# Performance work log

Hardware: AMD Instinct MI355X
Metric: run time of the kernel (lower is better)

Reference implementation:

```python
import jax, jax.numpy as jnp
import numpy as np

NUM_HEADS = 12


def setup_inputs() -> dict:
    key = jax.random.key(0)
    k1, k2, k3 = jax.random.split(key, 3)
    B, N, C = 2, 2048, 768
    x = jax.random.normal(k1, (B, N, C), dtype=jnp.float32)
    # torch nn.Linear weights: [out_features, in_features]
    w_qkv = jax.random.normal(k2, (3 * C, C), dtype=jnp.float32) * (C ** -0.5)
    w_mlp = jax.random.normal(k3, (C, C), dtype=jnp.float32) * (C ** -0.5)
    b_mlp = jnp.zeros((C,), dtype=jnp.float32)
    return {"x": x, "w_qkv": w_qkv, "w_mlp": w_mlp, "b_mlp": b_mlp}


def reference(x, w_qkv, w_mlp, b_mlp):
    B, N, C = x.shape
    H = NUM_HEADS
    hd = C // H
    scale = hd ** -0.5
    # qkv linear (no bias), then the module's reshape: [B,N,H,3,hd]
    qkv = (x @ w_qkv.T).reshape(B, N, H, 3, hd)
    # permute(3,0,2,1,4) -> q,k,v each [B,H,N,hd]
    q = jnp.transpose(qkv[:, :, :, 0, :], (0, 2, 1, 3))
    k = jnp.transpose(qkv[:, :, :, 1, :], (0, 2, 1, 3))
    v = jnp.transpose(qkv[:, :, :, 2, :], (0, 2, 1, 3))
    attn = jax.nn.softmax(jnp.einsum('bhqd,bhkd->bhqk', q, k) * scale, axis=-1)
    out = jnp.einsum('bhqk,bhkd->bhqd', attn, v)          # [B,H,N,hd]
    out = jnp.transpose(out, (0, 2, 1, 3)).reshape(B, N, C)
    return out @ w_mlp.T + b_mlp
```

## Files before the change

### kernel.cpp

```cpp
#include <hip/hip_runtime.h>
#include <math.h>

typedef unsigned short u16;
typedef unsigned int   u32;
typedef __attribute__((ext_vector_type(8))) short s8v;
typedef __attribute__((ext_vector_type(4))) float f4v;
typedef __attribute__((ext_vector_type(16))) float f16v;

#define NHEADS 12
#define SEQ 2048
#define CD 768
#define BB 2
#define QKVD 2304
#define CEXP 0.18033688f
#define DEFER_THR 44.0f

__device__ inline u16 f2bf(float f) {
    union { float f; unsigned u; } v; v.f = f;
    unsigned r = v.u + 0x7FFFu + ((v.u >> 16) & 1u);
    return (u16)(r >> 16);
}
__device__ inline u32 cvtpk_bf16(float lo, float hi) {
    u32 r;
    asm("v_cvt_pk_bf16_f32 %0, %1, %2" : "=v"(r) : "v"(lo), "v"(hi));
    return r;
}
__device__ inline float exp2_fast(float x) {
    float r;
    asm("v_exp_f32 %0, %1" : "=v"(r) : "v"(x));
    return r;
}
__device__ inline float max3f(float a, float b, float c) {
    float r;
    asm("v_max3_f32 %0, %1, %2, %3" : "=v"(r) : "v"(a), "v"(b), "v"(c));
    return r;
}

#define GLOAD16(SRC, DST) __builtin_amdgcn_global_load_lds(                 \
    (const __attribute__((address_space(1))) void*)(SRC),                   \
    (__attribute__((address_space(3))) void*)(DST), 16, 0, 0)

#define SW(r, c) ((((r) << 6) + (c)) ^ (((r) & 7) << 3))
#define SW16(r, c) ((((r) << 7) + (c)) ^ (((r) & 15) << 3))

__global__ __launch_bounds__(256)
void cvt3_kernel(const float* __restrict__ a, u16* __restrict__ oa, int na,
                 const float* __restrict__ b, u16* __restrict__ ob, int nb,
                 const float* __restrict__ c, u16* __restrict__ oc) {
    const int i = (blockIdx.x * 256 + threadIdx.x) * 8;
    const float* src; u16* dst;
    if (i < na)           { src = a + i;            dst = oa + i; }
    else if (i < na + nb) { src = b + (i - na);     dst = ob + (i - na); }
    else                  { src = c + (i - na - nb); dst = oc + (i - na - nb); }
    const float4 x = *(const float4*)src;
    const float4 y = *(const float4*)(src + 4);
    s8v o;
    o[0] = (short)f2bf(x.x); o[1] = (short)f2bf(x.y);
    o[2] = (short)f2bf(x.z); o[3] = (short)f2bf(x.w);
    o[4] = (short)f2bf(y.x); o[5] = (short)f2bf(y.y);
    o[6] = (short)f2bf(y.z); o[7] = (short)f2bf(y.w);
    *(s8v*)dst = o;
}

template<int BN, int NBX, bool OUT_BF16, bool BIAS>
__global__ __launch_bounds__(256)
void gemm_bf16(const u16* __restrict__ A, const u16* __restrict__ W,
               const float* __restrict__ bias, void* __restrict__ Cout,
               int M, int N, int K) {
    constexpr int NF = BN / 32;
    __shared__ u16 As[8192];
    __shared__ u16 Bs[BN * 64];
    const int tid = threadIdx.x;
    const int l  = tid & 63, w = tid >> 6;
    const int wr = w >> 1, wc = w & 1;
    const int lq = l & 15, lg = l >> 4;

    const int fid = blockIdx.x;
    const int cpx = gridDim.x >> 3;
    const int swz = (fid & 7) * cpx + (fid >> 3);
    const int rowBase = (swz / NBX) << 7;
    const int colBase = (swz % NBX) * BN;

    f4v acc[4][NF];
    #pragma unroll
    for (int m = 0; m < 4; ++m)
        #pragma unroll
        for (int n = 0; n < NF; ++n)
            #pragma unroll
            for (int r = 0; r < 4; ++r) acc[m][n][r] = 0.f;

    const int chunk = l & 7;
    const int r8    = l >> 3;

    for (int kb = 0; kb < K; kb += 64) {
        __syncthreads();
        #pragma unroll
        for (int j = 0; j < 4; ++j) {
            const int rowA = (w << 5) + (j << 3) + r8;
            const int sc   = (chunk ^ (rowA & 7)) << 3;
            GLOAD16(A + (size_t)(rowBase + rowA) * K + kb + sc,
                    &As[(w << 11) + (j << 9)]);
        }
        #pragma unroll
        for (int j = 0; j < NF; ++j) {
            const int rowB = w * (BN / 4) + (j << 3) + r8;
            const int sc   = (chunk ^ (rowB & 7)) << 3;
            GLOAD16(W + (size_t)(colBase + rowB) * K + kb + sc,
                    &Bs[w * (BN * 16) + (j << 9)]);
        }
        __syncthreads();
        #pragma unroll
        for (int h = 0; h < 2; ++h) {
            const int kc = (h << 5) + (lg << 3);
            s8v af[4], bf[NF];
            #pragma unroll
            for (int m = 0; m < 4; ++m)
                af[m] = *(const s8v*)&As[SW((wr << 6) + (m << 4) + lq, kc)];
            #pragma unroll
            for (int n = 0; n < NF; ++n)
                bf[n] = *(const s8v*)&Bs[SW(wc * (BN / 2) + (n << 4) + lq, kc)];
            #pragma unroll
            for (int m = 0; m < 4; ++m)
                #pragma unroll
                for (int n = 0; n < NF; ++n)
                    acc[m][n] = __builtin_amdgcn_mfma_f32_16x16x32_bf16(
                        af[m], bf[n], acc[m][n], 0, 0, 0);
        }
    }

    #pragma unroll
    for (int m = 0; m < 4; ++m)
        #pragma unroll
        for (int r = 0; r < 4; ++r) {
            const int row = rowBase + (wr << 6) + (m << 4) + (lg << 2) + r;
            #pragma unroll
            for (int n = 0; n < NF; ++n) {
                const int col = colBase + wc * (BN / 2) + (n << 4) + lq;
                float v = acc[m][n][r];
                if (BIAS) v += bias[col];
                if (OUT_BF16) ((u16*)Cout)[(size_t)row * N + col] = f2bf(v);
                else        ((float*)Cout)[(size_t)row * N + col] = v;
            }
        }
}

__global__ __launch_bounds__(256)
void vtrans_kernel(const u16* __restrict__ qkvb, u16* __restrict__ vT) {
    __shared__ u16 T[64][66];
    const int bh = blockIdx.y;
    const int tt = blockIdx.x;
    const int b = bh / NHEADS, h = bh % NHEADS;
    const int r  = threadIdx.x >> 2;
    const int dc = (threadIdx.x & 3) << 4;
    const u16* src = qkvb + (size_t)(b * SEQ + tt * 64 + r) * QKVD
                   + h * 192 + 128 + dc;
    *(s8v*)&T[r][dc]     = *(const s8v*)(src);
    *(s8v*)&T[r][dc + 8] = *(const s8v*)(src + 8);
    __syncthreads();
    const int d  = threadIdx.x >> 2;
    const int tc = (threadIdx.x & 3) << 4;
    s8v o0, o1;
    #pragma unroll
    for (int j = 0; j < 8; ++j) {
        o0[j] = (short)T[tc + j][d];
        o1[j] = (short)T[tc + 8 + j][d];
    }
    u16* dst = vT + ((size_t)bh * 64 + d) * SEQ + tt * 64 + tc;
    *(s8v*)dst = o0;
    *(s8v*)(dst + 8) = o1;
}

__global__ __launch_bounds__(256)
void attn_mfma(const u16* __restrict__ qkv, const u16* __restrict__ vT,
               u16* __restrict__ outb) {
    __shared__ u16 SL[20480];
    __shared__ float ML[128];
    const int tid = threadIdx.x;
    const int l  = tid & 63, w = tid >> 6;
    const int g  = w >> 1, wl = w & 1;
    const int lq = l & 31;
    const int lh = l >> 5;

    const int fid = blockIdx.x;
    const int swz = (fid & 7) * 96 + (fid >> 3);
    const int q0 = (swz & 31) << 6;
    const int bh = swz >> 5;
    const int b = bh / NHEADS, hh = bh % NHEADS;
    const u16* base  = qkv + (size_t)b * SEQ * QKVD + hh * 192;
    const u16* baseK = base + 64;
    const u16* vbh   = vT + (size_t)bh * 64 * SEQ;

    const int kv0 = g << 10;
    u16* Kl = SL + (g << 13);
    u16* Vl = Kl + 4096;
    u16* Ql = SL + 16384;
    float* Of32 = (float*)(SL + 8192);
    float* Msh = ML;
    float* Lsh = ML + 64;
    u16* Ot = SL + 16384;

    u32 kso[4], vso[4];
    #pragma unroll
    for (int i = 0; i < 4; ++i) {
        const int r  = (wl << 4) + (i << 2) + (l >> 4);
        const int cg = (l & 15) ^ (r & 15);
        const int kk = ((cg >> 3) << 5) + r;
        const int cc = (cg & 7) << 3;
        kso[i] = (u32)((kv0 + kk) * QKVD + cc);
        vso[i] = (u32)(kk * SEQ + kv0 + cc);
    }

    {
        #pragma unroll
        for (int i = 0; i < 4; ++i) {
            GLOAD16(baseK + kso[i], &Kl[(wl << 11) + (i << 9)]);
            GLOAD16(vbh  + vso[i], &Vl[(wl << 11) + (i << 9)]);
        }
        const int qr = tid >> 3, qc = (tid & 7) << 3;
        const s8v qv0 = *(const s8v*)(base + (size_t)(q0 + qr) * QKVD + qc);
        const s8v qv1 = *(const s8v*)(base + (size_t)(q0 + 32 + qr) * QKVD + qc);
        *(s8v*)&Ql[SW16(qr, qc)]      = qv0;
        *(s8v*)&Ql[SW16(qr, 64 + qc)] = qv1;
    }
    __syncthreads();

    s8v qf[4];
    #pragma unroll
    for (int ds = 0; ds < 4; ++ds)
        qf[ds] = *(const s8v*)&Ql[SW16(lq, (wl << 6) + (ds << 4) + (lh << 3))];

    f16v z16;
    #pragma unroll
    for (int r = 0; r < 16; ++r) z16[r] = 0.f;
    f16v oa0 = z16, oa1 = z16;
    float osum = 0.f, mrun = -3.0e38f;

    for (int t = 0; t < 16; ++t) {
        s8v ka[8];
        #pragma unroll
        for (int kb = 0; kb < 2; ++kb)
            #pragma unroll
            for (int ds = 0; ds < 4; ++ds)
                ka[kb * 4 + ds] = *(const s8v*)
                    &Kl[SW16(lq, (kb << 6) + (ds << 4) + (lh << 3))];
        f16v s0 = z16, s1 = z16;
        __builtin_amdgcn_s_setprio(1);
        #pragma unroll
        for (int ds = 0; ds < 4; ++ds)
            s0 = __builtin_amdgcn_mfma_f32_32x32x16_bf16(ka[ds], qf[ds], s0, 0, 0, 0);
        #pragma unroll
        for (int ds = 0; ds < 4; ++ds)
            s1 = __builtin_amdgcn_mfma_f32_32x32x16_bf16(ka[4 + ds], qf[ds], s1, 0, 0, 0);
        __builtin_amdgcn_s_setprio(0);

        __syncthreads();
        if (t < 15) {
            const u16* sb = baseK + (size_t)(t + 1) * (64 * QKVD);
            #pragma unroll
            for (int i = 0; i < 4; ++i)
                GLOAD16(sb + kso[i], &Kl[(wl << 11) + (i << 9)]);
        }

        float mxa = max3f(s0[0], s0[1], s0[2]);
        mxa = max3f(mxa, s0[3], s0[4]);  mxa = max3f(mxa, s0[5], s0[6]);
        mxa = max3f(mxa, s0[7], s0[8]);  mxa = max3f(mxa, s0[9], s0[10]);
        mxa = max3f(mxa, s0[11], s0[12]); mxa = max3f(mxa, s0[13], s0[14]);
        float mxb = max3f(s1[0], s1[1], s1[2]);
        mxb = max3f(mxb, s1[3], s1[4]);  mxb = max3f(mxb, s1[5], s1[6]);
        mxb = max3f(mxb, s1[7], s1[8]);  mxb = max3f(mxb, s1[9], s1[10]);
        mxb = max3f(mxb, s1[11], s1[12]); mxb = max3f(mxb, s1[13], s1[14]);
        float mx = max3f(mxa, s0[15], mxb);
        mx = fmaxf(mx, s1[15]);
        if (!__all(mx <= mrun + DEFER_THR)) {
            mx = fmaxf(mx, __shfl_xor(mx, 32));
            const float mn = fmaxf(mrun, mx);
            const float al = exp2_fast((mrun - mn) * CEXP);
            mrun = mn;
            #pragma unroll
            for (int r = 0; r < 16; ++r) { oa0[r] *= al; oa1[r] *= al; }
            osum *= al;
        }
        const float mC = -mrun * CEXP;
        #pragma unroll
        for (int r = 0; r < 16; ++r) {
            s0[r] = exp2_fast(fmaf(s0[r], CEXP, mC));
            s1[r] = exp2_fast(fmaf(s1[r], CEXP, mC));
        }
        {
            float a0 = s0[0] + s0[4], a1 = s0[1] + s0[5];
            float a2 = s0[2] + s0[6], a3 = s0[3] + s0[7];
            a0 += s0[8] + s0[12];  a1 += s0[9] + s0[13];
            a2 += s0[10] + s0[14]; a3 += s0[11] + s0[15];
            a0 += s1[0] + s1[4];   a1 += s1[1] + s1[5];
            a2 += s1[2] + s1[6];   a3 += s1[3] + s1[7];
            a0 += s1[8] + s1[12];  a1 += s1[9] + s1[13];
            a2 += s1[10] + s1[14]; a3 += s1[11] + s1[15];
            osum += (a0 + a1) + (a2 + a3);
        }

        s8v pf[4];
        #pragma unroll
        for (int s = 0; s < 2; ++s) {
            u32 A0 = cvtpk_bf16(s0[8*s+0], s0[8*s+1]);
            u32 B0 = cvtpk_bf16(s0[8*s+4], s0[8*s+5]);
            u32 A1 = cvtpk_bf16(s0[8*s+2], s0[8*s+3]);
            u32 B1 = cvtpk_bf16(s0[8*s+6], s0[8*s+7]);
            asm volatile("v_permlane32_swap_b32 %0, %1" : "+v"(A0), "+v"(B0));
            asm volatile("v_permlane32_swap_b32 %0, %1" : "+v"(A1), "+v"(B1));
            union { s8v v; u32 u[4]; } pu;
            pu.u[0] = A0; pu.u[1] = A1; pu.u[2] = B0; pu.u[3] = B1;
            pf[s] = pu.v;
        }
        #pragma unroll
        for (int s = 0; s < 2; ++s) {
            u32 A0 = cvtpk_bf16(s1[8*s+0], s1[8*s+1]);
            u32 B0 = cvtpk_bf16(s1[8*s+4], s1[8*s+5]);
            u32 A1 = cvtpk_bf16(s1[8*s+2], s1[8*s+3]);
            u32 B1 = cvtpk_bf16(s1[8*s+6], s1[8*s+7]);
            asm volatile("v_permlane32_swap_b32 %0, %1" : "+v"(A0), "+v"(B0));
            asm volatile("v_permlane32_swap_b32 %0, %1" : "+v"(A1), "+v"(B1));
            union { s8v v; u32 u[4]; } pu;
            pu.u[0] = A0; pu.u[1] = A1; pu.u[2] = B0; pu.u[3] = B1;
            pf[2 + s] = pu.v;
        }

        s8v va[8];
        #pragma unroll
        for (int db = 0; db < 2; ++db)
            #pragma unroll
            for (int ks = 0; ks < 4; ++ks)
                va[db * 4 + ks] = *(const s8v*)
                    &Vl[SW16(lq, (db << 6) + (ks << 4) + (lh << 3))];
        __builtin_amdgcn_s_setprio(1);
        #pragma unroll
        for (int ks = 0; ks < 4; ++ks)
            oa0 = __builtin_amdgcn_mfma_f32_32x32x16_bf16(va[ks], pf[ks], oa0, 0, 0, 0);
        #pragma unroll
        for (int ks = 0; ks < 4; ++ks)
            oa1 = __builtin_amdgcn_mfma_f32_32x32x16_bf16(va[4 + ks], pf[ks], oa1, 0, 0, 0);
        __builtin_amdgcn_s_setprio(0);

        __syncthreads();
        if (t < 15) {
            const u16* sb = vbh + (t + 1) * 64;
            #pragma unroll
            for (int i = 0; i < 4; ++i)
                GLOAD16(sb + vso[i], &Vl[(wl << 11) + (i << 9)]);
        }
    }

    const float osum_t = osum + __shfl_xor(osum, 32);
    const int wq = (wl << 5) + lq;
    if (g == 1) {
        if (lh == 0) { Msh[wq] = mrun; Lsh[wq] = osum_t; }
        #pragma unroll
        for (int r = 0; r < 16; ++r) {
            const int d0 = (r & 3) + ((r >> 2) << 3) + (lh << 2);
            Of32[d0 * 64 + wq]        = oa0[r];
            Of32[(d0 + 32) * 64 + wq] = oa1[r];
        }
    }
    __syncthreads();
    if (g == 0) {
        const float m1 = Msh[wq], l1 = Lsh[wq];
        const float M  = fmaxf(mrun, m1);
        const float w0 = exp2_fast((mrun - M) * CEXP);
        const float w1 = exp2_fast((m1 - M) * CEXP);
        const float inv = 1.f / (osum_t * w0 + l1 * w1);
        const float a0 = w0 * inv, a1 = w1 * inv;
        #pragma unroll
        for (int j = 0; j < 4; ++j) {
            const int d0 = (j << 3) + (lh << 2);
            const float v0 = oa0[4*j+0] * a0 + Of32[(d0+0)*64+wq] * a1;
            const float v1 = oa0[4*j+1] * a0 + Of32[(d0+1)*64+wq] * a1;
            const float v2 = oa0[4*j+2] * a0 + Of32[(d0+2)*64+wq] * a1;
            const float v3 = oa0[4*j+3] * a0 + Of32[(d0+3)*64+wq] * a1;
            *(u32*)&Ot[SW(wq, d0)]     = cvtpk_bf16(v0, v1);
            *(u32*)&Ot[SW(wq, d0 + 2)] = cvtpk_bf16(v2, v3);
            const float u0 = oa1[4*j+0] * a0 + Of32[(d0+32)*64+wq] * a1;
            const float u1 = oa1[4*j+1] * a0 + Of32[(d0+33)*64+wq] * a1;
            const float u2 = oa1[4*j+2] * a0 + Of32[(d0+34)*64+wq] * a1;
            const float u3 = oa1[4*j+3] * a0 + Of32[(d0+35)*64+wq] * a1;
            *(u32*)&Ot[SW(wq, d0 + 32)] = cvtpk_bf16(u0, u1);
            *(u32*)&Ot[SW(wq, d0 + 34)] = cvtpk_bf16(u2, u3);
        }
    }
    __syncthreads();
    {
        const int row = tid >> 2, c0 = (tid & 3) << 4;
        const s8v o0 = *(const s8v*)&Ot[SW(row, c0)];
        const s8v o1 = *(const s8v*)&Ot[SW(row, c0 + 8)];
        u16* dst = outb + (size_t)(b * SEQ + q0 + row) * CD + hh * 64 + c0;
        *(s8v*)dst = o0;
        *(s8v*)(dst + 8) = o1;
    }
}

extern "C" void kernel_launch(void* const* d_in, const int* in_sizes, int n_in,
                              void* d_out, int out_size, void* d_ws, size_t ws_size,
                              hipStream_t stream) {
    const float* x     = (const float*)d_in[0];
    const float* w_qkv = (const float*)d_in[1];
    const float* w_mlp = (const float*)d_in[2];
    const float* b_mlp = (const float*)d_in[3];
    float* out = (float*)d_out;

    const int NX  = BB * SEQ * CD;
    const int NWQ = QKVD * CD;
    const int NWM = CD * CD;
    const int NQK = BB * SEQ * QKVD;
    const int NAT = BB * SEQ * CD;
    u16* xb    = (u16*)d_ws;
    u16* wqkvb = xb + NX;
    u16* wmlpb = wqkvb + NWQ;
    u16* qkvb  = wmlpb + NWM;
    u16* attnb = qkvb + NQK;
    u16* vTb   = attnb + NAT;

    cvt3_kernel<<<(NX + NWQ + NWM) / 2048, 256, 0, stream>>>(
        x, xb, NX, w_qkv, wqkvb, NWQ, w_mlp, wmlpb);

    const int M = BB * SEQ;
    {
        gemm_bf16<128, 18, true, false><<<576, 256, 0, stream>>>(
            xb, wqkvb, nullptr, qkvb, M, QKVD, CD);
    }
    {
        dim3 grid(SEQ / 64, BB * NHEADS);
        vtrans_kernel<<<grid, 256, 0, stream>>>(qkvb, vTb);
    }
    {
        attn_mfma<<<768, 256, 0, stream>>>(qkvb, vTb, attnb);
    }
    {
        gemm_bf16<64, 12, false, true><<<384, 256, 0, stream>>>(
            attnb, wmlpb, b_mlp, out, M, CD, CD);
    }
}
```

Measured before the change: 98.42 us.

## Load K/V directly from global into registers with 8 waves splitting keys

The attention kernel drops its LDS staging of K, V and Q with global_load_lds and instead reads MFMA fragments straight from global memory into registers. The block grows to 512 threads so that four wave groups each handle a quarter of the key range. Their partial softmax states are then merged in a two-stage tree reduction through shared memory. This removes the per-iteration barriers and LDS traffic but relies on L1/L2 caching of uncoalesced per-lane global loads, and it adds reduction overhead.

```diff
diff --git a/kernel.cpp b/kernel.cpp
--- a/kernel.cpp
+++ b/kernel.cpp
@@ -41,7 +41,6 @@
     (__attribute__((address_space(3))) void*)(DST), 16, 0, 0)
 
 #define SW(r, c) ((((r) << 6) + (c)) ^ (((r) & 7) << 3))
-#define SW16(r, c) ((((r) << 7) + (c)) ^ (((r) & 15) << 3))
 
 __global__ __launch_bounds__(256)
 void cvt3_kernel(const float* __restrict__ a, u16* __restrict__ oa, int na,
@@ -170,16 +169,14 @@
     *(s8v*)(dst + 8) = o1;
 }
 
-__global__ __launch_bounds__(256)
+__global__ __launch_bounds__(512)
 void attn_mfma(const u16* __restrict__ qkv, const u16* __restrict__ vT,
                u16* __restrict__ outb) {
-    __shared__ u16 SL[20480];
-    __shared__ float ML[128];
+    __shared__ u16 SL[20992];
     const int tid = threadIdx.x;
     const int l  = tid & 63, w = tid >> 6;
-    const int g  = w >> 1, wl = w & 1;
-    const int lq = l & 31;
-    const int lh = l >> 5;
+    const int wl = w & 1, g = (w >> 1) & 1, tp = w >> 2;
+    const int lq = l & 31, lh = l >> 5;
 
     const int fid = blockIdx.x;
     const int swz = (fid & 7) * 96 + (fid >> 3);
@@ -190,44 +187,16 @@
     const u16* baseK = base + 64;
     const u16* vbh   = vT + (size_t)bh * 64 * SEQ;
 
-    const int kv0 = g << 10;
-    u16* Kl = SL + (g << 13);
-    u16* Vl = Kl + 4096;
-    u16* Ql = SL + 16384;
-    float* Of32 = (float*)(SL + 8192);
-    float* Msh = ML;
-    float* Lsh = ML + 64;
-    u16* Ot = SL + 16384;
-
-    u32 kso[4], vso[4];
-    #pragma unroll
-    for (int i = 0; i < 4; ++i) {
-        const int r  = (wl << 4) + (i << 2) + (l >> 4);
-        const int cg = (l & 15) ^ (r & 15);
-        const int kk = ((cg >> 3) << 5) + r;
-        const int cc = (cg & 7) << 3;
-        kso[i] = (u32)((kv0 + kk) * QKVD + cc);
-        vso[i] = (u32)(kk * SEQ + kv0 + cc);
-    }
-
-    {
-        #pragma unroll
-        for (int i = 0; i < 4; ++i) {
-            GLOAD16(baseK + kso[i], &Kl[(wl << 11) + (i << 9)]);
-            GLOAD16(vbh  + vso[i], &Vl[(wl << 11) + (i << 9)]);
-        }
-        const int qr = tid >> 3, qc = (tid & 7) << 3;
-        const s8v qv0 = *(const s8v*)(base + (size_t)(q0 + qr) * QKVD + qc);
-        const s8v qv1 = *(const s8v*)(base + (size_t)(q0 + 32 + qr) * QKVD + qc);
-        *(s8v*)&Ql[SW16(qr, qc)]      = qv0;
-        *(s8v*)&Ql[SW16(qr, 64 + qc)] = qv1;
-    }
-    __syncthreads();
+    float* slots = (float*)SL;
+    u16*  Ot    = SL + 16384;
+    float* stats = (float*)(SL + 20480);
+    const int sid = (wl << 1) + g;
 
     s8v qf[4];
     #pragma unroll
     for (int ds = 0; ds < 4; ++ds)
-        qf[ds] = *(const s8v*)&Ql[SW16(lq, (wl << 6) + (ds << 4) + (lh << 3))];
+        qf[ds] = *(const s8v*)(base + (size_t)(q0 + (wl << 5) + lq) * QKVD
+                               + (ds << 4) + (lh << 3));
 
     f16v z16;
     #pragma unroll
@@ -235,31 +204,28 @@
     f16v oa0 = z16, oa1 = z16;
     float osum = 0.f, mrun = -3.0e38f;
 
-    for (int t = 0; t < 16; ++t) {
-        s8v ka[8];
-        #pragma unroll
-        for (int kb = 0; kb < 2; ++kb)
-            #pragma unroll
-            for (int ds = 0; ds < 4; ++ds)
-                ka[kb * 4 + ds] = *(const s8v*)
-                    &Kl[SW16(lq, (kb << 6) + (ds << 4) + (lh << 3))];
+    for (int j = 0; j < 8; ++j) {
+        const int keyb = (g << 10) + (((j << 1) | tp) << 6);
+        const u16* kp = baseK + (size_t)(keyb + lq) * QKVD + (lh << 3);
+
+        s8v ka[4];
+        #pragma unroll
+        for (int ds = 0; ds < 4; ++ds)
+            ka[ds] = *(const s8v*)(kp + (ds << 4));
         f16v s0 = z16, s1 = z16;
         __builtin_amdgcn_s_setprio(1);
         #pragma unroll
         for (int ds = 0; ds < 4; ++ds)
             s0 = __builtin_amdgcn_mfma_f32_32x32x16_bf16(ka[ds], qf[ds], s0, 0, 0, 0);
+        __builtin_amdgcn_s_setprio(0);
         #pragma unroll
         for (int ds = 0; ds < 4; ++ds)
-            s1 = __builtin_amdgcn_mfma_f32_32x32x16_bf16(ka[4 + ds], qf[ds], s1, 0, 0, 0);
+            ka[ds] = *(const s8v*)(kp + (size_t)32 * QKVD + (ds << 4));
+        __builtin_amdgcn_s_setprio(1);
+        #pragma unroll
+        for (int ds = 0; ds < 4; ++ds)
+            s1 = __builtin_amdgcn_mfma_f32_32x32x16_bf16(ka[ds], qf[ds], s1, 0, 0, 0);
         __builtin_amdgcn_s_setprio(0);
-
-        __syncthreads();
-        if (t < 15) {
-            const u16* sb = baseK + (size_t)(t + 1) * (64 * QKVD);
-            #pragma unroll
-            for (int i = 0; i < 4; ++i)
-                GLOAD16(sb + kso[i], &Kl[(wl << 11) + (i << 9)]);
-        }
 
         float mxa = max3f(s0[0], s0[1], s0[2]);
         mxa = max3f(mxa, s0[3], s0[4]);  mxa = max3f(mxa, s0[5], s0[6]);
@@ -324,75 +290,99 @@
             pf[2 + s] = pu.v;
         }
 
-        s8v va[8];
-        #pragma unroll
-        for (int db = 0; db < 2; ++db)
-            #pragma unroll
-            for (int ks = 0; ks < 4; ++ks)
-                va[db * 4 + ks] = *(const s8v*)
-                    &Vl[SW16(lq, (db << 6) + (ks << 4) + (lh << 3))];
+        const u16* vp = vbh + (size_t)lq * SEQ + keyb + (lh << 3);
+        s8v va[4];
+        #pragma unroll
+        for (int ks = 0; ks < 4; ++ks)
+            va[ks] = *(const s8v*)(vp + (ks << 4));
         __builtin_amdgcn_s_setprio(1);
         #pragma unroll
         for (int ks = 0; ks < 4; ++ks)
             oa0 = __builtin_amdgcn_mfma_f32_32x32x16_bf16(va[ks], pf[ks], oa0, 0, 0, 0);
+        __builtin_amdgcn_s_setprio(0);
         #pragma unroll
         for (int ks = 0; ks < 4; ++ks)
-            oa1 = __builtin_amdgcn_mfma_f32_32x32x16_bf16(va[4 + ks], pf[ks], oa1, 0, 0, 0);
+            va[ks] = *(const s8v*)(vp + (size_t)32 * SEQ + (ks << 4));
+        __builtin_amdgcn_s_setprio(1);
+        #pragma unroll
+        for (int ks = 0; ks < 4; ++ks)
+            oa1 = __builtin_amdgcn_mfma_f32_32x32x16_bf16(va[ks], pf[ks], oa1, 0, 0, 0);
         __builtin_amdgcn_s_setprio(0);
-
-        __syncthreads();
-        if (t < 15) {
-            const u16* sb = vbh + (t + 1) * 64;
-            #pragma unroll
-            for (int i = 0; i < 4; ++i)
-                GLOAD16(sb + vso[i], &Vl[(wl << 11) + (i << 9)]);
-        }
-    }
-
-    const float osum_t = osum + __shfl_xor(osum, 32);
-    const int wq = (wl << 5) + lq;
-    if (g == 1) {
-        if (lh == 0) { Msh[wq] = mrun; Lsh[wq] = osum_t; }
+    }
+
+    float lsum = osum + __shfl_xor(osum, 32);
+
+    if (tp == 1) {
+        float* sp = slots + sid * 2048;
+        if (lh == 0) { stats[sid * 64 + lq] = mrun;
+                       stats[sid * 64 + 32 + lq] = lsum; }
         #pragma unroll
         for (int r = 0; r < 16; ++r) {
             const int d0 = (r & 3) + ((r >> 2) << 3) + (lh << 2);
-            Of32[d0 * 64 + wq]        = oa0[r];
-            Of32[(d0 + 32) * 64 + wq] = oa1[r];
+            sp[(d0 << 5) + lq]        = oa0[r];
+            sp[((d0 + 32) << 5) + lq] = oa1[r];
         }
     }
     __syncthreads();
-    if (g == 0) {
-        const float m1 = Msh[wq], l1 = Lsh[wq];
+    if (tp == 0) {
+        float* sp = slots + sid * 2048;
+        const float m1 = stats[sid * 64 + lq];
+        const float l1 = stats[sid * 64 + 32 + lq];
         const float M  = fmaxf(mrun, m1);
-        const float w0 = exp2_fast((mrun - M) * CEXP);
-        const float w1 = exp2_fast((m1 - M) * CEXP);
-        const float inv = 1.f / (osum_t * w0 + l1 * w1);
-        const float a0 = w0 * inv, a1 = w1 * inv;
-        #pragma unroll
-        for (int j = 0; j < 4; ++j) {
-            const int d0 = (j << 3) + (lh << 2);
-            const float v0 = oa0[4*j+0] * a0 + Of32[(d0+0)*64+wq] * a1;
-            const float v1 = oa0[4*j+1] * a0 + Of32[(d0+1)*64+wq] * a1;
-            const float v2 = oa0[4*j+2] * a0 + Of32[(d0+2)*64+wq] * a1;
-            const float v3 = oa0[4*j+3] * a0 + Of32[(d0+3)*64+wq] * a1;
+        const float wa = exp2_fast((mrun - M) * CEXP);
+        const float wb = exp2_fast((m1 - M) * CEXP);
+        mrun = M; lsum = lsum * wa + l1 * wb;
+        #pragma unroll
+        for (int r = 0; r < 16; ++r) {
+            const int d0 = (r & 3) + ((r >> 2) << 3) + (lh << 2);
+            oa0[r] = oa0[r] * wa + sp[(d0 << 5) + lq] * wb;
+            oa1[r] = oa1[r] * wa + sp[((d0 + 32) << 5) + lq] * wb;
+        }
+        if (g == 1) {
+            if (lh == 0) { stats[sid * 64 + lq] = mrun;
+                           stats[sid * 64 + 32 + lq] = lsum; }
+            #pragma unroll
+            for (int r = 0; r < 16; ++r) {
+                const int d0 = (r & 3) + ((r >> 2) << 3) + (lh << 2);
+                sp[(d0 << 5) + lq]        = oa0[r];
+                sp[((d0 + 32) << 5) + lq] = oa1[r];
+            }
+        }
+    }
+    __syncthreads();
+    if (tp == 0 && g == 0) {
+        const int sid2 = (wl << 1) + 1;
+        float* sp = slots + sid2 * 2048;
+        const float m1 = stats[sid2 * 64 + lq];
+        const float l1 = stats[sid2 * 64 + 32 + lq];
+        const float M  = fmaxf(mrun, m1);
+        const float wa = exp2_fast((mrun - M) * CEXP);
+        const float wb = exp2_fast((m1 - M) * CEXP);
+        const float inv = 1.f / (lsum * wa + l1 * wb);
+        const float a0 = wa * inv, a1 = wb * inv;
+        const int wq = (wl << 5) + lq;
+        #pragma unroll
+        for (int j2 = 0; j2 < 4; ++j2) {
+            const int d0 = (j2 << 3) + (lh << 2);
+            const float v0 = oa0[4*j2+0] * a0 + sp[((d0+0) << 5) + lq] * a1;
+            const float v1 = oa0[4*j2+1] * a0 + sp[((d0+1) << 5) + lq] * a1;
+            const float v2 = oa0[4*j2+2] * a0 + sp[((d0+2) << 5) + lq] * a1;
+            const float v3 = oa0[4*j2+3] * a0 + sp[((d0+3) << 5) + lq] * a1;
             *(u32*)&Ot[SW(wq, d0)]     = cvtpk_bf16(v0, v1);
             *(u32*)&Ot[SW(wq, d0 + 2)] = cvtpk_bf16(v2, v3);
-            const float u0 = oa1[4*j+0] * a0 + Of32[(d0+32)*64+wq] * a1;
-            const float u1 = oa1[4*j+1] * a0 + Of32[(d0+33)*64+wq] * a1;
-            const float u2 = oa1[4*j+2] * a0 + Of32[(d0+34)*64+wq] * a1;
-            const float u3 = oa1[4*j+3] * a0 + Of32[(d0+35)*64+wq] * a1;
+            const float u0 = oa1[4*j2+0] * a0 + sp[((d0+32) << 5) + lq] * a1;
+            const float u1 = oa1[4*j2+1] * a0 + sp[((d0+33) << 5) + lq] * a1;
+            const float u2 = oa1[4*j2+2] * a0 + sp[((d0+34) << 5) + lq] * a1;
+            const float u3 = oa1[4*j2+3] * a0 + sp[((d0+35) << 5) + lq] * a1;
             *(u32*)&Ot[SW(wq, d0 + 32)] = cvtpk_bf16(u0, u1);
             *(u32*)&Ot[SW(wq, d0 + 34)] = cvtpk_bf16(u2, u3);
         }
     }
     __syncthreads();
     {
-        const int row = tid >> 2, c0 = (tid & 3) << 4;
-        const s8v o0 = *(const s8v*)&Ot[SW(row, c0)];
-        const s8v o1 = *(const s8v*)&Ot[SW(row, c0 + 8)];
-        u16* dst = outb + (size_t)(b * SEQ + q0 + row) * CD + hh * 64 + c0;
-        *(s8v*)dst = o0;
-        *(s8v*)(dst + 8) = o1;
+        const int row = tid >> 3, c0 = (tid & 7) << 3;
+        const s8v o = *(const s8v*)&Ot[SW(row, c0)];
+        *(s8v*)(outb + (size_t)(b * SEQ + q0 + row) * CD + hh * 64 + c0) = o;
     }
 }
 
@@ -430,7 +420,7 @@
         vtrans_kernel<<<grid, 256, 0, stream>>>(qkvb, vTb);
     }
     {
-        attn_mfma<<<768, 256, 0, stream>>>(qkvb, vTb, attnb);
+        attn_mfma<<<768, 512, 0, stream>>>(qkvb, vTb, attnb);
     }
     {
         gemm_bf16<64, 12, false, true><<<384, 256, 0, stream>>>(
```

New measurement: 140.6 us. +42.9%, slower.
